# Optimization experiments

Hardware: AMD Instinct MI355X
Metric: run time of the kernel (lower is better)

The kernel has to match this reference:

```python
import jax, jax.numpy as jnp
import numpy as np

B, S, D = 4, 2048, 1024
MULT = 4
INNER = MULT * D
E = 4          # n_expert
K = 1          # top-k
ALPHA = 0.5


def setup_inputs() -> dict:
    key = jax.random.key(0)
    ks = jax.random.split(key, 8)
    std = 0.02
    x = jax.random.normal(ks[0], (B, S, D), jnp.float32)
    W1 = jax.random.normal(ks[1], (D, INNER), jnp.float32) * std
    b1 = jnp.zeros((INNER,), jnp.float32)
    W2 = jax.random.normal(ks[2], (INNER, D), jnp.float32) * std
    b2 = jnp.zeros((D,), jnp.float32)
    Wg = jax.random.normal(ks[3], (D, E), jnp.float32) * std
    ew1 = jax.random.normal(ks[4], (E, D, INNER), jnp.float32) * std
    ew3 = jax.random.normal(ks[5], (E, D, INNER), jnp.float32) * std
    ew2 = jax.random.normal(ks[6], (E, INNER, D), jnp.float32) * std
    return {"x": x, "W1": W1, "b1": b1, "W2": W2, "b2": b2,
            "Wg": Wg, "ew1": ew1, "ew3": ew3, "ew2": ew2}


def reference(x, W1, b1, W2, b2, Wg, ew1, ew3, ew2):
    # Dense branch: Linear -> GELU (exact, torch default) -> Linear
    y_dense = jax.nn.gelu(x @ W1 + b1, approximate=False) @ W2 + b2

    # MoE branch: top-k softmax routing, SwiGLU experts
    logits = x @ Wg                                   # [B,S,E]
    probs = jax.nn.softmax(logits, axis=-1)
    topv, topi = jax.lax.top_k(probs, K)              # [B,S,K]
    gates = topv / jnp.sum(topv, axis=-1, keepdims=True)  # renormalize top-k
    onehot = jax.nn.one_hot(topi, E, dtype=x.dtype)   # [B,S,K,E]
    combine = jnp.sum(gates[..., None] * onehot, axis=-2)  # [B,S,E]

    y_moe = jnp.zeros_like(x)
    for e in range(E):  # small fixed expert count
        h = jax.nn.silu(x @ ew1[e]) * (x @ ew3[e])    # [B,S,INNER]
        y_moe = y_moe + combine[..., e:e + 1] * (h @ ew2[e])

    # Load-balancing aux loss: E * sum_e f_e * P_e
    frac = jnp.mean(jnp.sum(onehot, axis=-2), axis=(0, 1)) / K  # [E]
    pmean = jnp.mean(probs, axis=(0, 1))                        # [E]
    aux = E * jnp.sum(frac * pmean)

    y = ALPHA * y_dense + (1.0 - ALPHA) * y_moe
    return (y, aux)
```

## Files before the change

kernel.cpp:

```cpp
#include <hip/hip_runtime.h>
#include <hip/hip_bf16.h>


static constexpr int MT = 8192;
static constexpr int DD = 1024;
static constexpr int DI = 4096;

typedef float f32x4 __attribute__((ext_vector_type(4)));
typedef __bf16 bf16x8 __attribute__((ext_vector_type(8)));
typedef unsigned short u16;

__device__ __forceinline__ u16 f2bf(float f) {
    union { __hip_bfloat16 b; u16 u; } v;
    v.b = __float2bfloat16(f);
    return v.u;
}
__device__ __forceinline__ float bf2f(u16 u) {
    union { float f; unsigned i; } v;
    v.i = ((unsigned)u) << 16;
    return v.f;
}

__device__ __forceinline__ void gload_lds16(const void* g, void* l) {
    __builtin_amdgcn_global_load_lds(
        (const __attribute__((address_space(1))) void*)g,
        (__attribute__((address_space(3))) void*)l, 16, 0, 0);
}

__device__ __forceinline__ float gelu_f(float v) {
    return 0.5f * v * (1.0f + erff(v * 0.70710678118654752f));
}
__device__ __forceinline__ float silu_f(float v) {
    return v / (1.0f + expf(-v));
}

#define FENCE() asm volatile("" ::: "memory")
#define BARRIER() do { FENCE(); __builtin_amdgcn_s_barrier(); FENCE(); } while (0)
#define WAIT_LGKM0() asm volatile("s_waitcnt lgkmcnt(0)" ::: "memory")

__device__ __forceinline__ void transpose_tile(
    const float* __restrict__ s, u16* __restrict__ d, int K, int N,
    int pack, int packOff) {
    __shared__ u16 t[64][72];
    int n0 = blockIdx.x * 64, k0 = blockIdx.y * 64;
    int tid = threadIdx.x;
    int c = tid & 15;
    int r = tid >> 4;
#pragma unroll
    for (int p = 0; p < 4; ++p) {
        int k = r + p * 16;
        float4 v = *(const float4*)(s + (size_t)(k0 + k) * N + n0 + c * 4);
        t[c * 4 + 0][k] = f2bf(v.x);
        t[c * 4 + 1][k] = f2bf(v.y);
        t[c * 4 + 2][k] = f2bf(v.z);
        t[c * 4 + 3][k] = f2bf(v.w);
    }
    __syncthreads();
    int n = tid >> 2, kc = (tid & 3) * 16;
    const uint4* p0 = (const uint4*)&t[n][kc];
    uint4 a = p0[0], b = p0[1];
    int gn = n0 + n;
    int dr = pack ? ((gn >> 5) * 64 + (gn & 31) + packOff) : gn;
    uint4* o = (uint4*)(d + (size_t)dr * K + k0 + kc);
    o[0] = a; o[1] = b;
}

__global__ void __launch_bounds__(256) transpose_up(
    const float* __restrict__ W1, const float* __restrict__ ew1,
    const float* __restrict__ ew3, u16* __restrict__ W1t,
    u16* __restrict__ ew13t) {
    int z = blockIdx.z;
    if (z == 0) {
        transpose_tile(W1, W1t, DD, DI, 0, 0);
    } else if (z <= 4) {
        transpose_tile(ew1 + (size_t)(z - 1) * DD * DI,
                       ew13t + (size_t)(z - 1) * 2 * DD * DI, DD, DI, 1, 0);
    } else {
        transpose_tile(ew3 + (size_t)(z - 5) * DD * DI,
                       ew13t + (size_t)(z - 5) * 2 * DD * DI, DD, DI, 1, 32);
    }
}

__global__ void __launch_bounds__(256) transpose_dn(
    const float* __restrict__ W2, const float* __restrict__ ew2,
    u16* __restrict__ W2t, u16* __restrict__ ew2t) {
    int z = blockIdx.z;
    if (z == 0) {
        transpose_tile(W2, W2t, DI, DD, 0, 0);
    } else {
        transpose_tile(ew2 + (size_t)(z - 1) * DI * DD,
                       ew2t + (size_t)(z - 1) * DI * DD, DI, DD, 0, 0);
    }
}

__global__ void __launch_bounds__(256) gate_kernel(
    const float* __restrict__ x, const float* __restrict__ Wg,
    float* __restrict__ psum_blk, int* __restrict__ expertA) {
    int w = threadIdx.x >> 6, l = threadIdx.x & 63;
    int t = blockIdx.x * 4 + w;
    const float* xr = x + (size_t)t * DD;
    double a0 = 0, a1 = 0, a2 = 0, a3 = 0;
#pragma unroll
    for (int i = 0; i < 4; ++i) {
        int k = i * 256 + l * 4;
        float4 xv = *(const float4*)(xr + k);
        float4 w0 = *(const float4*)(Wg + (size_t)(k + 0) * 4);
        float4 w1 = *(const float4*)(Wg + (size_t)(k + 1) * 4);
        float4 w2 = *(const float4*)(Wg + (size_t)(k + 2) * 4);
        float4 w3 = *(const float4*)(Wg + (size_t)(k + 3) * 4);
        a0 += (double)xv.x * w0.x + (double)xv.y * w1.x + (double)xv.z * w2.x + (double)xv.w * w3.x;
        a1 += (double)xv.x * w0.y + (double)xv.y * w1.y + (double)xv.z * w2.y + (double)xv.w * w3.y;
        a2 += (double)xv.x * w0.z + (double)xv.y * w1.z + (double)xv.z * w2.z + (double)xv.w * w3.z;
        a3 += (double)xv.x * w0.w + (double)xv.y * w1.w + (double)xv.z * w2.w + (double)xv.w * w3.w;
    }
#pragma unroll
    for (int o = 32; o; o >>= 1) {
        a0 += __shfl_down(a0, o); a1 += __shfl_down(a1, o);
        a2 += __shfl_down(a2, o); a3 += __shfl_down(a3, o);
    }
    __shared__ float wps[4][4];
    if (l == 0) {
        double lg[4] = {a0, a1, a2, a3};
        int best = 0;
#pragma unroll
        for (int e = 1; e < 4; ++e) if (lg[e] > lg[best]) best = e;
        double m = lg[best], s = 0, p[4];
#pragma unroll
        for (int e = 0; e < 4; ++e) { p[e] = exp(lg[e] - m); s += p[e]; }
#pragma unroll
        for (int e = 0; e < 4; ++e) wps[w][e] = (float)(p[e] / s);
        expertA[t] = best;
    }
    __syncthreads();
    if (threadIdx.x < 4)
        psum_blk[blockIdx.x * 4 + threadIdx.x] =
            wps[0][threadIdx.x] + wps[1][threadIdx.x] + wps[2][threadIdx.x] + wps[3][threadIdx.x];
}

__global__ void __launch_bounds__(1024) build_lists(
    const int* __restrict__ expertA, const float* __restrict__ psum_blk,
    int* __restrict__ dstArr, int* __restrict__ rev,
    int* __restrict__ offsets, float* __restrict__ auxOut) {
    __shared__ int sc[4][1024];
    __shared__ float fs[1024];
    __shared__ float psum_s[4];
    __shared__ int tot_s[4], off_s[4];
    int tid = threadIdx.x;
    int le[8]; int c[4] = {0, 0, 0, 0};
#pragma unroll
    for (int i = 0; i < 8; ++i) { int e = expertA[tid * 8 + i]; le[i] = e; c[e]++; }
#pragma unroll
    for (int e = 0; e < 4; ++e) sc[e][tid] = c[e];
    __syncthreads();
    for (int o = 1; o < 1024; o <<= 1) {
        int v[4];
#pragma unroll
        for (int e = 0; e < 4; ++e) v[e] = (tid >= o) ? sc[e][tid - o] : 0;
        __syncthreads();
#pragma unroll
        for (int e = 0; e < 4; ++e) if (tid >= o) sc[e][tid] += v[e];
        __syncthreads();
    }
    if (tid == 0) {
        int o = 0;
#pragma unroll
        for (int e = 0; e < 4; ++e) {
            tot_s[e] = sc[e][1023]; off_s[e] = o; offsets[e] = o; o += tot_s[e];
        }
        offsets[4] = o;
    }
    __syncthreads();
    int base[4];
#pragma unroll
    for (int e = 0; e < 4; ++e) base[e] = off_s[e] + sc[e][tid] - c[e];
#pragma unroll
    for (int i = 0; i < 8; ++i) {
        int e = le[i]; int d = base[e]++; int t = tid * 8 + i;
        dstArr[t] = d; rev[d] = t;
    }
    float ps[4];
#pragma unroll
    for (int e = 0; e < 4; ++e)
        ps[e] = psum_blk[(2 * tid) * 4 + e] + psum_blk[(2 * tid + 1) * 4 + e];
    for (int e = 0; e < 4; ++e) {
        fs[tid] = ps[e]; __syncthreads();
        for (int o = 512; o; o >>= 1) { if (tid < o) fs[tid] += fs[tid + o]; __syncthreads(); }
        if (tid == 0) psum_s[e] = fs[0];
        __syncthreads();
    }
    if (tid == 0) {
        float a = 0;
#pragma unroll
        for (int e = 0; e < 4; ++e)
            a += ((float)tot_s[e] * (1.f / 8192.f)) * (psum_s[e] * (1.f / 8192.f));
        auxOut[0] = 4.f * a;
    }
}

__global__ void __launch_bounds__(256) gather_kernel(
    const float* __restrict__ x, const int* __restrict__ dstArr,
    u16* __restrict__ xg) {
    int w = threadIdx.x >> 6, l = threadIdx.x & 63;
    int t = blockIdx.x * 4 + w;
    int dst = dstArr[t];
    const float* xr = x + (size_t)t * DD;
#pragma unroll
    for (int i = 0; i < 4; ++i) {
        int k = i * 256 + l * 4;
        float4 v = *(const float4*)(xr + k);
        ushort4 u;
        u.x = f2bf(v.x); u.y = f2bf(v.y); u.z = f2bf(v.z); u.w = f2bf(v.w);
        *(ushort4*)(xg + (size_t)dst * DD + k) = u;
    }
}

template <int MODE, int NF>
__global__ void __launch_bounds__(512, 2) gemm8(
    const u16* __restrict__ A, const u16* __restrict__ Bw,
    const float* __restrict__ bias,
    u16* __restrict__ outB, float* __restrict__ outF,
    const int* __restrict__ offsets, const int* __restrict__ rev,
    int N, int K) {
    constexpr int BN   = NF * 64;
    constexpr int WCW  = NF * 16;
    constexpr int AELT = 2 * 256 * 32;
    constexpr int BUFE = AELT + 2 * BN * 32;
    constexpr int NIB  = NF / 2;
    __shared__ u16 lds[2 * BUFE];

    const int tid = threadIdx.x;
    const int w = tid >> 6, l = tid & 63;
    const int lr = l & 15, lg = l >> 4;
    const int wr = w >> 2, wc = w & 3;

    int rowBase, rowsValid = 256;
    const u16* Bp = Bw;
    if constexpr (MODE >= 2) {
        int e = blockIdx.z;
        int off = offsets[e], cnt = offsets[e + 1] - off;
        if ((int)blockIdx.y * 256 >= cnt) return;
        rowBase = off + blockIdx.y * 256;
        rowsValid = cnt - (int)blockIdx.y * 256;
        if (rowsValid > 256) rowsValid = 256;
        Bp = Bw + (size_t)e * ((size_t)2 * DD * DI);
    } else {
        rowBase = blockIdx.y * 256;
    }
    const int colBase = blockIdx.x * BN;
    const int NT = K >> 6;

    auto stageA = [&](int kt, int b, int ks) {
        const int kk = (kt << 6) + (ks << 5);
#pragma unroll
        for (int i = 0; i < 2; ++i) {
            int o = ((w << 1) + i) * 512 + (l << 3);
            int o2 = o ^ (((o >> 8) & 1) << 4);
            gload_lds16(A + (size_t)(rowBase + (o2 >> 5)) * K + kk + (o2 & 31),
                        &lds[b * BUFE + ks * 8192 + ((w << 1) + i) * 512]);
        }
    };
    auto stageB = [&](int kt, int b, int ks) {
        const int kk = (kt << 6) + (ks << 5);
#pragma unroll
        for (int i = 0; i < NIB; ++i) {
            int o = (w * NIB + i) * 512 + (l << 3);
            int o2 = o ^ (((o >> 8) & 1) << 4);
            gload_lds16(Bp + (size_t)(colBase + (o2 >> 5)) * K + kk + (o2 & 31),
                        &lds[b * BUFE + AELT + ks * (BN * 32) + (w * NIB + i) * 512]);
        }
    };

#define WAIT_VMB() do { \
    if constexpr (NF == 4) asm volatile("s_waitcnt vmcnt(4)" ::: "memory"); \
    else                   asm volatile("s_waitcnt vmcnt(3)" ::: "memory"); \
} while (0)

#define READBF(b_, ks_) do { \
    _Pragma("unroll") \
    for (int n = 0; n < NF; ++n) { \
        int e_ = (wc * WCW + n * 16 + lr) * 32 + lg * 8; \
        e_ ^= ((e_ >> 8) & 1) << 4; \
        bf[n] = *(const bf16x8*)&lds[(b_) * BUFE + AELT + (ks_) * (BN * 32) + e_]; \
    } \
} while (0)

#define READAF(b_, ks_, mq_) do { \
    _Pragma("unroll") \
    for (int m = 0; m < 4; ++m) { \
        int e_ = (wr * 128 + ((mq_) * 4 + m) * 16 + lr) * 32 + lg * 8; \
        e_ ^= ((e_ >> 8) & 1) << 4; \
        af[m] = *(const bf16x8*)&lds[(b_) * BUFE + (ks_) * 8192 + e_]; \
    } \
} while (0)

#define DOMFMA(mq_) do { \
    __builtin_amdgcn_s_setprio(1); \
    _Pragma("unroll") \
    for (int m = 0; m < 4; ++m) \
    _Pragma("unroll") \
    for (int n = 0; n < NF; ++n) \
        acc[(mq_) * 4 + m][n] = __builtin_amdgcn_mfma_f32_16x16x32_bf16( \
            bf[n], af[m], acc[(mq_) * 4 + m][n], 0, 0, 0); \
    __builtin_amdgcn_s_setprio(0); \
} while (0)

    f32x4 acc[8][NF];
#pragma unroll
    for (int m = 0; m < 8; ++m)
#pragma unroll
        for (int n = 0; n < NF; ++n) acc[m][n] = (f32x4){0.f, 0.f, 0.f, 0.f};
    bf16x8 af[4], bf[NF];

    stageA(0, 0, 0); stageB(0, 0, 0); stageA(0, 0, 1); stageB(0, 0, 1);
    stageA(1, 1, 0); stageB(1, 1, 0);
    WAIT_VMB();
    BARRIER();

    for (int t = 0; t < NT; ++t) {
        const int cb = t & 1, nb = cb ^ 1;
        const int tp1 = (t + 1 < NT) ? t + 1 : NT - 1;
        const int tp2 = (t + 2 < NT) ? t + 2 : NT - 1;
        READBF(cb, 0); READAF(cb, 0, 0); stageA(tp1, nb, 1);
        BARRIER(); WAIT_LGKM0(); DOMFMA(0); BARRIER();
        READAF(cb, 0, 1); stageB(tp1, nb, 1);
        BARRIER(); WAIT_LGKM0(); DOMFMA(1); BARRIER();
        READBF(cb, 1); READAF(cb, 1, 0); stageA(tp2, cb, 0);
        BARRIER(); WAIT_LGKM0(); DOMFMA(0); BARRIER();
        READAF(cb, 1, 1); stageB(tp2, cb, 0);
        BARRIER(); WAIT_LGKM0(); DOMFMA(1);
        WAIT_VMB();
        BARRIER();
    }

#pragma unroll
    for (int m = 0; m < 8; ++m) {
        int rloc = wr * 128 + m * 16 + lr;
        if (MODE >= 2 && rloc >= rowsValid) continue;
        size_t grow = (size_t)(rowBase + rloc);
        if constexpr (MODE == 2) {
#pragma unroll
            for (int n = 0; n < 2; ++n) {
                int col = (colBase >> 1) + wc * 32 + n * 16 + lg * 4;
                f32x4 v1 = acc[m][n], v3 = acc[m][n + 2];
                ushort4 u;
                u.x = f2bf(silu_f(v1[0]) * v3[0]);
                u.y = f2bf(silu_f(v1[1]) * v3[1]);
                u.z = f2bf(silu_f(v1[2]) * v3[2]);
                u.w = f2bf(silu_f(v1[3]) * v3[3]);
                *(ushort4*)(outB + grow * N + col) = u;
            }
        } else {
#pragma unroll
            for (int n = 0; n < NF; ++n) {
                int col = colBase + wc * WCW + n * 16 + lg * 4;
                f32x4 v = acc[m][n];
                f32x4 bb = *(const f32x4*)(bias + col);
                ushort4 u;
                u.x = f2bf(gelu_f(v[0] + bb[0]));
                u.y = f2bf(gelu_f(v[1] + bb[1]));
                u.z = f2bf(gelu_f(v[2] + bb[2]));
                u.w = f2bf(gelu_f(v[3] + bb[3]));
                *(ushort4*)(outB + grow * N + col) = u;
            }
        }
    }
#undef WAIT_VMB
#undef READBF
#undef READAF
#undef DOMFMA
}

__global__ void __launch_bounds__(512, 2) gemm8dn(
    const u16* __restrict__ hd, const u16* __restrict__ hg,
    const u16* __restrict__ W2t, const u16* __restrict__ ew2t,
    u16* __restrict__ yA, float* __restrict__ y,
    const int* __restrict__ offsets, const int* __restrict__ rev) {
    constexpr int NF = 2;
    constexpr int BN = 128;
    constexpr int WCW = 32;
    constexpr int AELT = 2 * 256 * 32;
    constexpr int BUFE = AELT + 2 * BN * 32;
    __shared__ u16 lds[2 * BUFE];

    const int tid = threadIdx.x;
    const int w = tid >> 6, l = tid & 63;
    const int lr = l & 15, lg = l >> 4;
    const int wr = w >> 2, wc = w & 3;

    int wg = blockIdx.x;
    int c = wg & 7;
    int s = wg >> 3;
    int x = s & 7;
    int ps = c + ((s >> 3) << 3);
    bool dense = (ps >= 128);
    const u16* Ap;
    const u16* Bp;
    int rowBase, rowsValid = 256;
    if (dense) {
        rowBase = (ps - 128) << 8;
        Ap = hd; Bp = W2t;
    } else {
        int e = ps >> 5, yl = ps & 31;
        int off = offsets[e], cnt = offsets[e + 1] - off;
        if (yl * 256 >= cnt) return;
        rowBase = off + yl * 256;
        rowsValid = cnt - yl * 256;
        if (rowsValid > 256) rowsValid = 256;
        Ap = hg; Bp = ew2t + (size_t)e * DD * DI;
    }
    const int colBase = x * BN;
    const int NT = DI >> 6;

    auto stageA = [&](int kt, int b, int ks) {
        const int kk = (kt << 6) + (ks << 5);
#pragma unroll
        for (int i = 0; i < 2; ++i) {
            int o = ((w << 1) + i) * 512 + (l << 3);
            int o2 = o ^ (((o >> 8) & 1) << 4);
            gload_lds16(Ap + (size_t)(rowBase + (o2 >> 5)) * DI + kk + (o2 & 31),
                        &lds[b * BUFE + ks * 8192 + ((w << 1) + i) * 512]);
        }
    };
    auto stageB = [&](int kt, int b, int ks) {
        const int kk = (kt << 6) + (ks << 5);
        int o = w * 512 + (l << 3);
        int o2 = o ^ (((o >> 8) & 1) << 4);
        gload_lds16(Bp + (size_t)(colBase + (o2 >> 5)) * DI + kk + (o2 & 31),
                    &lds[b * BUFE + AELT + ks * (BN * 32) + w * 512]);
    };

#define WAIT_VMB() asm volatile("s_waitcnt vmcnt(3)" ::: "memory")
#define READBF(b_, ks_) do { \
    _Pragma("unroll") \
    for (int n = 0; n < NF; ++n) { \
        int e_ = (wc * WCW + n * 16 + lr) * 32 + lg * 8; \
        e_ ^= ((e_ >> 8) & 1) << 4; \
        bf[n] = *(const bf16x8*)&lds[(b_) * BUFE + AELT + (ks_) * (BN * 32) + e_]; \
    } \
} while (0)
#define READAF(b_, ks_, mq_) do { \
    _Pragma("unroll") \
    for (int m = 0; m < 4; ++m) { \
        int e_ = (wr * 128 + ((mq_) * 4 + m) * 16 + lr) * 32 + lg * 8; \
        e_ ^= ((e_ >> 8) & 1) << 4; \
        af[m] = *(const bf16x8*)&lds[(b_) * BUFE + (ks_) * 8192 + e_]; \
    } \
} while (0)
#define DOMFMA(mq_) do { \
    __builtin_amdgcn_s_setprio(1); \
    _Pragma("unroll") \
    for (int m = 0; m < 4; ++m) \
    _Pragma("unroll") \
    for (int n = 0; n < NF; ++n) \
        acc[(mq_) * 4 + m][n] = __builtin_amdgcn_mfma_f32_16x16x32_bf16( \
            bf[n], af[m], acc[(mq_) * 4 + m][n], 0, 0, 0); \
    __builtin_amdgcn_s_setprio(0); \
} while (0)

    f32x4 acc[8][NF];
#pragma unroll
    for (int m = 0; m < 8; ++m)
#pragma unroll
        for (int n = 0; n < NF; ++n) acc[m][n] = (f32x4){0.f, 0.f, 0.f, 0.f};
    bf16x8 af[4], bf[NF];

    stageA(0, 0, 0); stageB(0, 0, 0); stageA(0, 0, 1); stageB(0, 0, 1);
    stageA(1, 1, 0); stageB(1, 1, 0);
    WAIT_VMB();
    BARRIER();

    for (int t = 0; t < NT; ++t) {
        const int cb = t & 1, nb = cb ^ 1;
        const int tp1 = (t + 1 < NT) ? t + 1 : NT - 1;
        const int tp2 = (t + 2 < NT) ? t + 2 : NT - 1;
        READBF(cb, 0); READAF(cb, 0, 0); stageA(tp1, nb, 1);
        BARRIER(); WAIT_LGKM0(); DOMFMA(0); BARRIER();
        READAF(cb, 0, 1); stageB(tp1, nb, 1);
        BARRIER(); WAIT_LGKM0(); DOMFMA(1); BARRIER();
        READBF(cb, 1); READAF(cb, 1, 0); stageA(tp2, cb, 0);
        BARRIER(); WAIT_LGKM0(); DOMFMA(0); BARRIER();
        READAF(cb, 1, 1); stageB(tp2, cb, 0);
        BARRIER(); WAIT_LGKM0(); DOMFMA(1);
        WAIT_VMB();
        BARRIER();
    }

#pragma unroll
    for (int m = 0; m < 8; ++m) {
        int rloc = wr * 128 + m * 16 + lr;
        if (!dense && rloc >= rowsValid) continue;
        int r = rowBase + rloc;
#pragma unroll
        for (int n = 0; n < NF; ++n) {
            int col = colBase + wc * WCW + n * 16 + lg * 4;
            f32x4 v = acc[m][n];
            if (dense) {
                ushort4 u;
                u.x = f2bf(v[0]); u.y = f2bf(v[1]);
                u.z = f2bf(v[2]); u.w = f2bf(v[3]);
                *(ushort4*)(yA + (size_t)r * DD + col) = u;
            } else {
                int tok = rev[r];
                f32x4 rr;
#pragma unroll
                for (int j = 0; j < 4; ++j) rr[j] = 0.5f * v[j];
                *(f32x4*)(y + (size_t)tok * DD + col) = rr;
            }
        }
    }
#undef WAIT_VMB
#undef READBF
#undef READAF
#undef DOMFMA
}

__global__ void __launch_bounds__(256) combine_kernel(
    const u16* __restrict__ yA, const float* __restrict__ b2,
    const int* __restrict__ rev, float* __restrict__ y) {
    int w = threadIdx.x >> 6, l = threadIdx.x & 63;
    int r = blockIdx.x * 4 + w;
    int tok = rev[r];
    const u16* ar = yA + (size_t)r * DD;
    float* yr = y + (size_t)tok * DD;
#pragma unroll
    for (int i = 0; i < 4; ++i) {
        int c = i * 256 + l * 4;
        ushort4 ua = *(const ushort4*)(ar + c);
        float4 bb = *(const float4*)(b2 + c);
        f32x4 o = *(f32x4*)(yr + c);
        o[0] += 0.5f * (bf2f(ua.x) + bb.x);
        o[1] += 0.5f * (bf2f(ua.y) + bb.y);
        o[2] += 0.5f * (bf2f(ua.z) + bb.z);
        o[3] += 0.5f * (bf2f(ua.w) + bb.w);
        *(f32x4*)(yr + c) = o;
    }
}

extern "C" void kernel_launch(void* const* d_in, const int* in_sizes, int n_in,
                              void* d_out, int out_size, void* d_ws, size_t ws_size,
                              hipStream_t stream) {
    const float* x   = (const float*)d_in[0];
    const float* W1  = (const float*)d_in[1];
    const float* b1  = (const float*)d_in[2];
    const float* W2  = (const float*)d_in[3];
    const float* b2  = (const float*)d_in[4];
    const float* Wg  = (const float*)d_in[5];
    const float* ew1 = (const float*)d_in[6];
    const float* ew3 = (const float*)d_in[7];
    const float* ew2 = (const float*)d_in[8];
    float* y = (float*)d_out;
    float* auxOut = y + (size_t)MT * DD;

    char* ws = (char*)d_ws;
    size_t off = 0;
    auto take = [&](size_t b) -> void* {
        void* p = ws + off;
        off += (b + 255) & ~(size_t)255;
        return p;
    };
    u16* W1t   = (u16*)take((size_t)DI * DD * 2);
    u16* W2t   = (u16*)take((size_t)DI * DD * 2);
    u16* ew2t  = (u16*)take((size_t)4 * DI * DD * 2);
    u16* xg    = (u16*)take((size_t)(MT + 256) * DD * 2);
    u16* hg    = (u16*)take((size_t)(MT + 256) * DI * 2);
    int* expertA  = (int*)take(MT * 4);
    int* dstArr   = (int*)take(MT * 4);
    int* revA     = (int*)take(MT * 4);
    float* psum_blk = (float*)take(2048 * 4 * 4);
    int* offsets  = (int*)take(64);
    size_t ew13Bytes = (size_t)4 * 2 * DI * DD * 2;
    size_t hdBytes   = (size_t)(MT + 256) * DI * 2;
    u16* ew13t = (u16*)take(ew13Bytes > hdBytes ? ew13Bytes : hdBytes);
    u16* hd    = ew13t;
    u16* yA = xg;

    if (ws_size < off) return;

    dim3 blk(256);
    transpose_up<<<dim3(DI / 64, DD / 64, 9), blk, 0, stream>>>(W1, ew1, ew3, W1t, ew13t);
    transpose_dn<<<dim3(DD / 64, DI / 64, 5), blk, 0, stream>>>(W2, ew2, W2t, ew2t);
    gate_kernel<<<2048, 256, 0, stream>>>(x, Wg, psum_blk, expertA);
    build_lists<<<1, 1024, 0, stream>>>(expertA, psum_blk, dstArr, revA, offsets, auxOut);
    gather_kernel<<<2048, 256, 0, stream>>>(x, dstArr, xg);
    gemm8<2, 4><<<dim3(2 * DI / 256, MT / 256, 4), dim3(512), 0, stream>>>(
        xg, ew13t, nullptr, hg, nullptr, offsets, nullptr, DI, DD);
    gemm8<0, 4><<<dim3(DI / 256, MT / 256), dim3(512), 0, stream>>>(
        xg, W1t, b1, hd, nullptr, nullptr, nullptr, DI, DD);
    gemm8dn<<<dim3(1280), dim3(512), 0, stream>>>(
        hd, hg, W2t, ew2t, yA, y, offsets, revA);
    combine_kernel<<<2048, blk, 0, stream>>>(yA, b2, revA, y);
}
```

Measured before the change: 574.2 us.

## Fuse dense and expert down-projections into one K-concatenated GEMM, drop combine kernel

```diff
diff --git a/kernel.cpp b/kernel.cpp
--- a/kernel.cpp
+++ b/kernel.cpp
@@ -14,11 +14,6 @@
     union { __hip_bfloat16 b; u16 u; } v;
     v.b = __float2bfloat16(f);
     return v.u;
-}
-__device__ __forceinline__ float bf2f(u16 u) {
-    union { float f; unsigned i; } v;
-    v.i = ((unsigned)u) << 16;
-    return v.f;
 }
 
 __device__ __forceinline__ void gload_lds16(const void* g, void* l) {
@@ -373,13 +368,14 @@
 __global__ void __launch_bounds__(512, 2) gemm8dn(
     const u16* __restrict__ hd, const u16* __restrict__ hg,
     const u16* __restrict__ W2t, const u16* __restrict__ ew2t,
-    u16* __restrict__ yA, float* __restrict__ y,
+    const float* __restrict__ b2, float* __restrict__ y,
     const int* __restrict__ offsets, const int* __restrict__ rev) {
-    constexpr int NF = 2;
-    constexpr int BN = 128;
-    constexpr int WCW = 32;
+    constexpr int NF   = 4;
+    constexpr int BN   = 256;
+    constexpr int WCW  = 64;
     constexpr int AELT = 2 * 256 * 32;
     constexpr int BUFE = AELT + 2 * BN * 32;
+    constexpr int NIB  = 2;
     __shared__ u16 lds[2 * BUFE];
 
     const int tid = threadIdx.x;
@@ -387,32 +383,19 @@
     const int lr = l & 15, lg = l >> 4;
     const int wr = w >> 2, wc = w & 3;
 
-    int wg = blockIdx.x;
-    int c = wg & 7;
-    int s = wg >> 3;
-    int x = s & 7;
-    int ps = c + ((s >> 3) << 3);
-    bool dense = (ps >= 128);
-    const u16* Ap;
-    const u16* Bp;
-    int rowBase, rowsValid = 256;
-    if (dense) {
-        rowBase = (ps - 128) << 8;
-        Ap = hd; Bp = W2t;
-    } else {
-        int e = ps >> 5, yl = ps & 31;
-        int off = offsets[e], cnt = offsets[e + 1] - off;
-        if (yl * 256 >= cnt) return;
-        rowBase = off + yl * 256;
-        rowsValid = cnt - yl * 256;
-        if (rowsValid > 256) rowsValid = 256;
-        Ap = hg; Bp = ew2t + (size_t)e * DD * DI;
-    }
-    const int colBase = x * BN;
-    const int NT = DI >> 6;
+    const int e = blockIdx.z;
+    const int off = offsets[e], cnt = offsets[e + 1] - off;
+    if ((int)blockIdx.y * 256 >= cnt) return;
+    const int rowBase = off + blockIdx.y * 256;
+    int rowsValid = cnt - (int)blockIdx.y * 256;
+    if (rowsValid > 256) rowsValid = 256;
+    const int colBase = blockIdx.x * BN;
+    const u16* Bm = ew2t + (size_t)e * DD * DI;
+    constexpr int NT = (2 * DI) >> 6;
 
     auto stageA = [&](int kt, int b, int ks) {
-        const int kk = (kt << 6) + (ks << 5);
+        const u16* Ap = (kt >= 64) ? hg : hd;
+        const int kk = ((kt & 63) << 6) + (ks << 5);
 #pragma unroll
         for (int i = 0; i < 2; ++i) {
             int o = ((w << 1) + i) * 512 + (l << 3);
@@ -422,14 +405,18 @@
         }
     };
     auto stageB = [&](int kt, int b, int ks) {
-        const int kk = (kt << 6) + (ks << 5);
-        int o = w * 512 + (l << 3);
-        int o2 = o ^ (((o >> 8) & 1) << 4);
-        gload_lds16(Bp + (size_t)(colBase + (o2 >> 5)) * DI + kk + (o2 & 31),
-                    &lds[b * BUFE + AELT + ks * (BN * 32) + w * 512]);
+        const u16* Bp = (kt >= 64) ? Bm : W2t;
+        const int kk = ((kt & 63) << 6) + (ks << 5);
+#pragma unroll
+        for (int i = 0; i < NIB; ++i) {
+            int o = (w * NIB + i) * 512 + (l << 3);
+            int o2 = o ^ (((o >> 8) & 1) << 4);
+            gload_lds16(Bp + (size_t)(colBase + (o2 >> 5)) * DI + kk + (o2 & 31),
+                        &lds[b * BUFE + AELT + ks * (BN * 32) + (w * NIB + i) * 512]);
+        }
     };
 
-#define WAIT_VMB() asm volatile("s_waitcnt vmcnt(3)" ::: "memory")
+#define WAIT_VMB() asm volatile("s_waitcnt vmcnt(4)" ::: "memory")
 #define READBF(b_, ks_) do { \
     _Pragma("unroll") \
     for (int n = 0; n < NF; ++n) { \
@@ -488,52 +475,23 @@
 #pragma unroll
     for (int m = 0; m < 8; ++m) {
         int rloc = wr * 128 + m * 16 + lr;
-        if (!dense && rloc >= rowsValid) continue;
-        int r = rowBase + rloc;
+        if (rloc >= rowsValid) continue;
+        int tok = rev[rowBase + rloc];
 #pragma unroll
         for (int n = 0; n < NF; ++n) {
             int col = colBase + wc * WCW + n * 16 + lg * 4;
             f32x4 v = acc[m][n];
-            if (dense) {
-                ushort4 u;
-                u.x = f2bf(v[0]); u.y = f2bf(v[1]);
-                u.z = f2bf(v[2]); u.w = f2bf(v[3]);
-                *(ushort4*)(yA + (size_t)r * DD + col) = u;
-            } else {
-                int tok = rev[r];
-                f32x4 rr;
-#pragma unroll
-                for (int j = 0; j < 4; ++j) rr[j] = 0.5f * v[j];
-                *(f32x4*)(y + (size_t)tok * DD + col) = rr;
-            }
+            f32x4 bb = *(const f32x4*)(b2 + col);
+            f32x4 r;
+#pragma unroll
+            for (int j = 0; j < 4; ++j) r[j] = 0.5f * (v[j] + bb[j]);
+            *(f32x4*)(y + (size_t)tok * DD + col) = r;
         }
     }
 #undef WAIT_VMB
 #undef READBF
 #undef READAF
 #undef DOMFMA
-}
-
-__global__ void __launch_bounds__(256) combine_kernel(
-    const u16* __restrict__ yA, const float* __restrict__ b2,
-    const int* __restrict__ rev, float* __restrict__ y) {
-    int w = threadIdx.x >> 6, l = threadIdx.x & 63;
-    int r = blockIdx.x * 4 + w;
-    int tok = rev[r];
-    const u16* ar = yA + (size_t)r * DD;
-    float* yr = y + (size_t)tok * DD;
-#pragma unroll
-    for (int i = 0; i < 4; ++i) {
-        int c = i * 256 + l * 4;
-        ushort4 ua = *(const ushort4*)(ar + c);
-        float4 bb = *(const float4*)(b2 + c);
-        f32x4 o = *(f32x4*)(yr + c);
-        o[0] += 0.5f * (bf2f(ua.x) + bb.x);
-        o[1] += 0.5f * (bf2f(ua.y) + bb.y);
-        o[2] += 0.5f * (bf2f(ua.z) + bb.z);
-        o[3] += 0.5f * (bf2f(ua.w) + bb.w);
-        *(f32x4*)(yr + c) = o;
-    }
 }
 
 extern "C" void kernel_launch(void* const* d_in, const int* in_sizes, int n_in,
@@ -572,7 +530,6 @@
     size_t hdBytes   = (size_t)(MT + 256) * DI * 2;
     u16* ew13t = (u16*)take(ew13Bytes > hdBytes ? ew13Bytes : hdBytes);
     u16* hd    = ew13t;
-    u16* yA = xg;
 
     if (ws_size < off) return;
 
@@ -586,7 +543,6 @@
         xg, ew13t, nullptr, hg, nullptr, offsets, nullptr, DI, DD);
     gemm8<0, 4><<<dim3(DI / 256, MT / 256), dim3(512), 0, stream>>>(
         xg, W1t, b1, hd, nullptr, nullptr, nullptr, DI, DD);
-    gemm8dn<<<dim3(1280), dim3(512), 0, stream>>>(
-        hd, hg, W2t, ew2t, yA, y, offsets, revA);
-    combine_kernel<<<2048, blk, 0, stream>>>(yA, b2, revA, y);
-}
+    gemm8dn<<<dim3(DD / 256, MT / 256, 4), dim3(512), 0, stream>>>(
+        hd, hg, W2t, ew2t, b2, y, offsets, revA);
+}
```

Measured after the change: 573.1 us. Within noise of the previous version (-0.2%).
